# Kernel tuning notes

Hardware: AMD Instinct MI355X
Metric: run time of the kernel (lower is better)

## Reference

```python
import jax, jax.numpy as jnp
import numpy as np

N = 50000       # nodes
E = 1200000     # edges (before self-loops)
IN_CH = 128
HID = 64
L = 3           # FAConv layers
EPS_RES = 0.1   # FAConv eps residual weight
BN_EPS = 1e-5


def _bn(x, g, b):
    # BatchNorm1d, training-mode statistics (biased variance, like torch)
    mu = x.mean(axis=0)
    var = x.var(axis=0)
    return g * (x - mu) * jax.lax.rsqrt(var + BN_EPS) + b


def setup_inputs() -> dict:
    key = jax.random.key(0)
    ks = jax.random.split(key, 12)
    s = lambda d: 1.0 / np.sqrt(d)
    H2 = HID // 2
    return {
        "x": jax.random.normal(ks[0], (N, IN_CH), jnp.float32),
        "edge_index": jax.random.randint(ks[1], (2, E), 0, N, dtype=jnp.int32),
        "batch_size": 10000,
        "W_in": jax.random.normal(ks[2], (IN_CH, HID), jnp.float32) * s(IN_CH),
        "b_in": jnp.zeros((HID,), jnp.float32),
        "att_l": jax.random.normal(ks[3], (L, HID), jnp.float32) * s(HID),
        "att_r": jax.random.normal(ks[4], (L, HID), jnp.float32) * s(HID),
        "bn_g": jnp.ones((L, HID), jnp.float32),
        "bn_b": jnp.zeros((L, HID), jnp.float32),
        "W1": jax.random.normal(ks[5], (HID, HID), jnp.float32) * s(HID),
        "b1": jnp.zeros((HID,), jnp.float32),
        "g1": jnp.ones((HID,), jnp.float32),
        "be1": jnp.zeros((HID,), jnp.float32),
        "W2": jax.random.normal(ks[6], (HID, H2), jnp.float32) * s(HID),
        "b2": jnp.zeros((H2,), jnp.float32),
        "g2": jnp.ones((H2,), jnp.float32),
        "be2": jnp.zeros((H2,), jnp.float32),
        "W3": jax.random.normal(ks[7], (H2, 1), jnp.float32) * s(H2),
        "b3": jnp.zeros((1,), jnp.float32),
    }


def reference(x, edge_index, batch_size, W_in, b_in, att_l, att_r, bn_g, bn_b,
              W1, b1, g1, be1, W2, b2, g2, be2, W3, b3):
    n = x.shape[0]
    # gcn_norm with self-loops (same for all layers since graph is fixed)
    loops = jnp.arange(n, dtype=edge_index.dtype)
    src = jnp.concatenate([edge_index[0], loops])  # j (source)
    dst = jnp.concatenate([edge_index[1], loops])  # i (target)
    deg = jax.ops.segment_sum(jnp.ones_like(dst, dtype=x.dtype), dst, num_segments=n)
    dinv = jnp.where(deg > 0, jax.lax.rsqrt(deg), 0.0)
    norm = dinv[src] * dinv[dst]                   # [E+N]

    x0 = jax.nn.relu(x @ W_in + b_in)              # [N, HID]
    h = x0
    for l in range(L):
        al = h @ att_l[l]                          # [N] att_l^T x
        ar = h @ att_r[l]                          # [N] att_r^T x
        alpha = jnp.tanh(al[src] + ar[dst])        # [E+N] signed attention
        msg = h[src] * (alpha * norm)[:, None]     # gather + weight
        out = jax.ops.segment_sum(msg, dst, num_segments=n) + EPS_RES * x0
        h = _bn(jax.nn.relu(out), bn_g[l], bn_b[l])

    z = h[:batch_size]
    z = jax.nn.relu(_bn(z @ W1 + b1, g1, be1))
    z = jax.nn.relu(_bn(z @ W2 + b2, g2, be2))
    return (z @ W3 + b3).squeeze(-1)
```

## Files before the change

kernel.cpp:

```cpp
#include <hip/hip_runtime.h>
#include <hip/hip_bf16.h>
#include <math.h>

#define NND 50000
#define NE  1200000
#define TOT (NE + NND)
#define INCH 128
#define HID 64
#define H2  32
#define NL  3
#define BSZ 10000
#define NB  196
#define NHB 128
#define NSTAT 256
#define CHUNK 4096
#define EPS_RES 0.1f
#define BN_EPS 1e-5f

typedef unsigned short ushort8v __attribute__((ext_vector_type(8)));

__device__ __forceinline__ float b2f(unsigned short u) {
    return __uint_as_float((unsigned)u << 16);
}

__device__ __forceinline__ float fast_tanh(float x) {
    float cx = fminf(fmaxf(x, -8.f), 8.f);
    float e = __expf(2.f * cx);
    return 1.f - __fdividef(2.f, e + 1.f);
}


__global__ __launch_bounds__(256) void bhist_kernel(const int* __restrict__ dst, int* __restrict__ bh_part, int ne) {
    __shared__ int arr[256];
    arr[threadIdx.x] = 0;
    __syncthreads();
    int i = blockIdx.x * 256 + threadIdx.x;
    int stride = gridDim.x * 256;
    for (int e = i; e < ne; e += stride) atomicAdd(&arr[dst[e] >> 8], 1);
    __syncthreads();
    bh_part[blockIdx.x * 256 + threadIdx.x] = arr[threadIdx.x];
}

__global__ __launch_bounds__(256) void bscan_kernel(const int* __restrict__ bh_part,
                                                    int* __restrict__ bstart, int* __restrict__ bcur,
                                                    int* __restrict__ offsets) {
    __shared__ int ls[256];
    int t = threadIdx.x;
    int v = 0;
    for (int k = 0; k < NHB; k++) v += bh_part[k * 256 + t];
    ls[t] = v;
    __syncthreads();
    for (int off = 1; off < 256; off <<= 1) {
        int tv = (t >= off) ? ls[t - off] : 0;
        __syncthreads();
        ls[t] += tv;
        __syncthreads();
    }
    int excl = ls[t] - v;
    if (t < NB) { bstart[t] = excl; bcur[t] = excl; }
    if (t == NB) bstart[NB] = ls[NB - 1];
    if (t == 0) offsets[NND] = TOT;
}

__global__ __launch_bounds__(256) void passA_kernel(const int* __restrict__ src, const int* __restrict__ dst,
                                                    int* __restrict__ bcur, unsigned* __restrict__ ebuf, int ne) {
    __shared__ int arr[256];
    int t = threadIdx.x;
    int base = blockIdx.x * CHUNK;
    int lim = min(base + CHUNK, ne);
    arr[t] = 0;
    __syncthreads();
    for (int e = base + t; e < lim; e += 256) atomicAdd(&arr[dst[e] >> 8], 1);
    __syncthreads();
    int cnt_t = arr[t];
    int claimed = 0;
    if (cnt_t > 0) claimed = atomicAdd(&bcur[t], cnt_t);
    __syncthreads();
    arr[t] = claimed;
    __syncthreads();
    for (int e = base + t; e < lim; e += 256) {
        int d = dst[e];
        int pos = atomicAdd(&arr[d >> 8], 1);
        ebuf[pos] = ((unsigned)src[e] << 8) | (unsigned)(d & 255);
    }
}

__global__ __launch_bounds__(256) void bucket_build_kernel(const unsigned* __restrict__ ebuf, const int* __restrict__ bstart,
                                                           int* __restrict__ offsets, int* __restrict__ csr,
                                                           float* __restrict__ aldi_f) {
    __shared__ int dcnt[256];
    __shared__ int ls[256];
    __shared__ int cur[256];
    int b = blockIdx.x, t = threadIdx.x;
    dcnt[t] = 0;
    __syncthreads();
    int beg = bstart[b], end = bstart[b + 1];
    for (int p = beg + t; p < end; p += 256) atomicAdd(&dcnt[ebuf[p] & 255u], 1);
    __syncthreads();
    int node = b * 256 + t;
    bool valid = node < NND;
    int d = valid ? (dcnt[t] + 1) : 0;
    ls[t] = d;
    __syncthreads();
    for (int off = 1; off < 256; off <<= 1) {
        int tv = (t >= off) ? ls[t - off] : 0;
        __syncthreads();
        ls[t] += tv;
        __syncthreads();
    }
    int off = bstart[b] + b * 256 + ls[t] - d;
    if (valid) {
        offsets[node] = off;
        aldi_f[2 * node + 1] = rsqrtf((float)d);
        csr[off] = node;
        cur[t] = off + 1;
    }
    __syncthreads();
    for (int p = beg + t; p < end; p += 256) {
        unsigned ed = ebuf[p];
        int pos = atomicAdd(&cur[ed & 255u], 1);
        csr[pos] = (int)(ed >> 8);
    }
}

__global__ __launch_bounds__(256) void gemm_in_kernel(const float* __restrict__ x, const float* __restrict__ W,
                                                      const float* __restrict__ b,
                                                      const float* __restrict__ attl, const float* __restrict__ attr,
                                                      __hip_bfloat16* __restrict__ x0bf,
                                                      float* __restrict__ aldi_f, float* __restrict__ ar) {
    __shared__ float Wl[INCH * HID];
    __shared__ float xs[16 * INCH];
    int t = threadIdx.x;
    for (int i = t; i < INCH * HID; i += 256) Wl[i] = W[i];
    size_t rowbase = (size_t)blockIdx.x * 16;
    for (int i = t; i < 16 * INCH; i += 256) xs[i] = x[rowbase * INCH + i];
    __syncthreads();
    int col = t & 63, rg = t >> 6;
    float a0 = 0.f, a1 = 0.f, a2 = 0.f, a3 = 0.f;
    for (int k = 0; k < INCH; k++) {
        float wk = Wl[k * HID + col];
        a0 = fmaf(xs[(rg * 4 + 0) * INCH + k], wk, a0);
        a1 = fmaf(xs[(rg * 4 + 1) * INCH + k], wk, a1);
        a2 = fmaf(xs[(rg * 4 + 2) * INCH + k], wk, a2);
        a3 = fmaf(xs[(rg * 4 + 3) * INCH + k], wk, a3);
    }
    float bb = b[col];
    a0 = fmaxf(a0 + bb, 0.f); a1 = fmaxf(a1 + bb, 0.f);
    a2 = fmaxf(a2 + bb, 0.f); a3 = fmaxf(a3 + bb, 0.f);
    size_t r = rowbase + rg * 4;
    x0bf[(r + 0) * HID + col] = __float2bfloat16(a0);
    x0bf[(r + 1) * HID + col] = __float2bfloat16(a1);
    x0bf[(r + 2) * HID + col] = __float2bfloat16(a2);
    x0bf[(r + 3) * HID + col] = __float2bfloat16(a3);
    float wl = attl[col], wr = attr[col];
    float p0 = a0 * wl, q0 = a0 * wr, p1 = a1 * wl, q1 = a1 * wr;
    float p2 = a2 * wl, q2 = a2 * wr, p3 = a3 * wl, q3 = a3 * wr;
    for (int off = 32; off > 0; off >>= 1) {
        p0 += __shfl_xor(p0, off); q0 += __shfl_xor(q0, off);
        p1 += __shfl_xor(p1, off); q1 += __shfl_xor(q1, off);
        p2 += __shfl_xor(p2, off); q2 += __shfl_xor(q2, off);
        p3 += __shfl_xor(p3, off); q3 += __shfl_xor(q3, off);
    }
    if (col == 0) {
        aldi_f[2 * (r + 0)] = p0; ar[r + 0] = q0;
        aldi_f[2 * (r + 1)] = p1; ar[r + 1] = q1;
        aldi_f[2 * (r + 2)] = p2; ar[r + 2] = q2;
        aldi_f[2 * (r + 3)] = p3; ar[r + 3] = q3;
    }
}

__global__ __launch_bounds__(256) void aggregate_kernel(const __hip_bfloat16* __restrict__ hbf,
                                                        const __hip_bfloat16* __restrict__ x0bf,
                                                        const float2* __restrict__ aldi,
                                                        const float* __restrict__ ar,
                                                        const int* __restrict__ offsets, const int* __restrict__ csr,
                                                        float* __restrict__ y, int n) {
    int v = (blockIdx.x * 256 + threadIdx.x) >> 6;
    int lane = threadIdx.x & 63;
    if (v >= n) return;
    int g = lane >> 3;
    int cl = (lane & 7) << 3;
    int beg = offsets[v], end = offsets[v + 1];
    float arv = ar[v];
    const unsigned short* hb = (const unsigned short*)hbf;
    float a0 = 0.f, a1 = 0.f, a2 = 0.f, a3 = 0.f, a4 = 0.f, a5 = 0.f, a6 = 0.f, a7 = 0.f;
    for (int base = beg; base < end; base += 64) {
        int p = base + lane;
        int u = 0; float c = 0.f;
        if (p < end) {
            u = csr[p];
            float2 ad = aldi[u];
            c = fast_tanh(ad.x + arv) * ad.y;
        }
        int cnt = min(64, end - base);
        int nchunk = (cnt + 31) >> 5;
        for (int ch = 0; ch < nchunk; ++ch) {
            int j0 = (ch << 5) + g;
            int j1 = j0 + 8, j2 = j0 + 16, j3 = j0 + 24;
            int js0 = (j0 < cnt) ? j0 : 0;
            int js1 = (j1 < cnt) ? j1 : 0;
            int js2 = (j2 < cnt) ? j2 : 0;
            int js3 = (j3 < cnt) ? j3 : 0;
            int u0 = __shfl(u, js0); float c0 = __shfl(c, js0); if (j0 >= cnt) c0 = 0.f;
            int u1 = __shfl(u, js1); float c1 = __shfl(c, js1); if (j1 >= cnt) c1 = 0.f;
            int u2 = __shfl(u, js2); float c2 = __shfl(c, js2); if (j2 >= cnt) c2 = 0.f;
            int u3 = __shfl(u, js3); float c3 = __shfl(c, js3); if (j3 >= cnt) c3 = 0.f;
            ushort8v h0 = *(const ushort8v*)(hb + (size_t)u0 * HID + cl);
            ushort8v h1 = *(const ushort8v*)(hb + (size_t)u1 * HID + cl);
            ushort8v h2 = *(const ushort8v*)(hb + (size_t)u2 * HID + cl);
            ushort8v h3 = *(const ushort8v*)(hb + (size_t)u3 * HID + cl);
            a0 = fmaf(b2f(h0[0]), c0, a0); a1 = fmaf(b2f(h0[1]), c0, a1);
            a2 = fmaf(b2f(h0[2]), c0, a2); a3 = fmaf(b2f(h0[3]), c0, a3);
            a4 = fmaf(b2f(h0[4]), c0, a4); a5 = fmaf(b2f(h0[5]), c0, a5);
            a6 = fmaf(b2f(h0[6]), c0, a6); a7 = fmaf(b2f(h0[7]), c0, a7);
            a0 = fmaf(b2f(h1[0]), c1, a0); a1 = fmaf(b2f(h1[1]), c1, a1);
            a2 = fmaf(b2f(h1[2]), c1, a2); a3 = fmaf(b2f(h1[3]), c1, a3);
            a4 = fmaf(b2f(h1[4]), c1, a4); a5 = fmaf(b2f(h1[5]), c1, a5);
            a6 = fmaf(b2f(h1[6]), c1, a6); a7 = fmaf(b2f(h1[7]), c1, a7);
            a0 = fmaf(b2f(h2[0]), c2, a0); a1 = fmaf(b2f(h2[1]), c2, a1);
            a2 = fmaf(b2f(h2[2]), c2, a2); a3 = fmaf(b2f(h2[3]), c2, a3);
            a4 = fmaf(b2f(h2[4]), c2, a4); a5 = fmaf(b2f(h2[5]), c2, a5);
            a6 = fmaf(b2f(h2[6]), c2, a6); a7 = fmaf(b2f(h2[7]), c2, a7);
            a0 = fmaf(b2f(h3[0]), c3, a0); a1 = fmaf(b2f(h3[1]), c3, a1);
            a2 = fmaf(b2f(h3[2]), c3, a2); a3 = fmaf(b2f(h3[3]), c3, a3);
            a4 = fmaf(b2f(h3[4]), c3, a4); a5 = fmaf(b2f(h3[5]), c3, a5);
            a6 = fmaf(b2f(h3[6]), c3, a6); a7 = fmaf(b2f(h3[7]), c3, a7);
        }
    }
    for (int off = 8; off < 64; off <<= 1) {
        a0 += __shfl_xor(a0, off); a1 += __shfl_xor(a1, off);
        a2 += __shfl_xor(a2, off); a3 += __shfl_xor(a3, off);
        a4 += __shfl_xor(a4, off); a5 += __shfl_xor(a5, off);
        a6 += __shfl_xor(a6, off); a7 += __shfl_xor(a7, off);
    }
    if (g == 0) {
        float dv = aldi[v].y;
        ushort8v xb = *(const ushort8v*)((const unsigned short*)x0bf + (size_t)v * HID + cl);
        float4 o0, o1;
        o0.x = fmaxf(fmaf(EPS_RES, b2f(xb[0]), a0 * dv), 0.f);
        o0.y = fmaxf(fmaf(EPS_RES, b2f(xb[1]), a1 * dv), 0.f);
        o0.z = fmaxf(fmaf(EPS_RES, b2f(xb[2]), a2 * dv), 0.f);
        o0.w = fmaxf(fmaf(EPS_RES, b2f(xb[3]), a3 * dv), 0.f);
        o1.x = fmaxf(fmaf(EPS_RES, b2f(xb[4]), a4 * dv), 0.f);
        o1.y = fmaxf(fmaf(EPS_RES, b2f(xb[5]), a5 * dv), 0.f);
        o1.z = fmaxf(fmaf(EPS_RES, b2f(xb[6]), a6 * dv), 0.f);
        o1.w = fmaxf(fmaf(EPS_RES, b2f(xb[7]), a7 * dv), 0.f);
        *(float4*)(y + (size_t)v * HID + cl) = o0;
        *(float4*)(y + (size_t)v * HID + cl + 4) = o1;
    }
}

template <int C>
__global__ __launch_bounds__(256) void bn_stats_fused_kernel(const float* __restrict__ y, int rows,
                                                             const float* __restrict__ g, const float* __restrict__ b,
                                                             float rows_inv,
                                                             float* __restrict__ acc, int* __restrict__ counter,
                                                             float* __restrict__ scale, float* __restrict__ shift) {
    const int TPR = C / 4;
    const int RPW = 64 / TPR;
    int lane = threadIdx.x & 63;
    int wave = threadIdx.x >> 6;
    int cl = (lane % TPR) * 4;
    int rsub = lane / TPR;
    int rpb = 4 * RPW;
    int r = blockIdx.x * rpb + wave * RPW + rsub;
    int stride = gridDim.x * rpb;
    float s0 = 0.f, s1 = 0.f, s2 = 0.f, s3 = 0.f, q0 = 0.f, q1 = 0.f, q2 = 0.f, q3 = 0.f;
    for (; r < rows; r += stride) {
        float4 v = *(const float4*)(y + (size_t)r * C + cl);
        s0 += v.x; q0 = fmaf(v.x, v.x, q0);
        s1 += v.y; q1 = fmaf(v.y, v.y, q1);
        s2 += v.z; q2 = fmaf(v.z, v.z, q2);
        s3 += v.w; q3 = fmaf(v.w, v.w, q3);
    }
    for (int off = TPR; off < 64; off <<= 1) {
        s0 += __shfl_xor(s0, off); q0 += __shfl_xor(q0, off);
        s1 += __shfl_xor(s1, off); q1 += __shfl_xor(q1, off);
        s2 += __shfl_xor(s2, off); q2 += __shfl_xor(q2, off);
        s3 += __shfl_xor(s3, off); q3 += __shfl_xor(q3, off);
    }
    __shared__ float lsum[4][64], lsq[4][64];
    if (lane < TPR) {
        lsum[wave][cl + 0] = s0; lsq[wave][cl + 0] = q0;
        lsum[wave][cl + 1] = s1; lsq[wave][cl + 1] = q1;
        lsum[wave][cl + 2] = s2; lsq[wave][cl + 2] = q2;
        lsum[wave][cl + 3] = s3; lsq[wave][cl + 3] = q3;
    }
    __syncthreads();
    int t = threadIdx.x;
    if (t < C) {
        float ts = lsum[0][t] + lsum[1][t] + lsum[2][t] + lsum[3][t];
        float tq = lsq[0][t] + lsq[1][t] + lsq[2][t] + lsq[3][t];
        atomicAdd(&acc[t], ts);
        atomicAdd(&acc[64 + t], tq);
    }
    __shared__ int islast;
    __syncthreads();
    if (t == 0) {
        __threadfence();
        int old = atomicAdd(counter, 1);
        islast = (old == (int)gridDim.x - 1) ? 1 : 0;
    }
    __syncthreads();
    if (islast && t < C) {
        float ts = atomicAdd(&acc[t], 0.f);
        float tq = atomicAdd(&acc[64 + t], 0.f);
        float mean = ts * rows_inv;
        float var = tq * rows_inv - mean * mean;
        float sc = g[t] * rsqrtf(var + BN_EPS);
        scale[t] = sc;
        shift[t] = b[t] - mean * sc;
    }
}

__global__ __launch_bounds__(256) void bn_fused_apply_attn_kernel(const float* __restrict__ y, int rows,
                                                                  const float* __restrict__ g, const float* __restrict__ b,
                                                                  float rows_inv,
                                                                  float* __restrict__ acc, int* __restrict__ counter,
                                                                  const float* __restrict__ attl, const float* __restrict__ attr,
                                                                  __hip_bfloat16* __restrict__ hbf,
                                                                  float* __restrict__ aldi_f, float* __restrict__ ar) {
    const int TPR = 16;
    int lane = threadIdx.x & 63;
    int wave = threadIdx.x >> 6;
    int cl = (lane % TPR) * 4;
    int rsub = lane / TPR;
    int r = blockIdx.x * 16 + wave * 4 + rsub;
    int stride = gridDim.x * 16;
    float s0 = 0.f, s1 = 0.f, s2 = 0.f, s3 = 0.f, q0 = 0.f, q1 = 0.f, q2 = 0.f, q3 = 0.f;
    for (; r < rows; r += stride) {
        float4 v = *(const float4*)(y + (size_t)r * HID + cl);
        s0 += v.x; q0 = fmaf(v.x, v.x, q0);
        s1 += v.y; q1 = fmaf(v.y, v.y, q1);
        s2 += v.z; q2 = fmaf(v.z, v.z, q2);
        s3 += v.w; q3 = fmaf(v.w, v.w, q3);
    }
    for (int off = TPR; off < 64; off <<= 1) {
        s0 += __shfl_xor(s0, off); q0 += __shfl_xor(q0, off);
        s1 += __shfl_xor(s1, off); q1 += __shfl_xor(q1, off);
        s2 += __shfl_xor(s2, off); q2 += __shfl_xor(q2, off);
        s3 += __shfl_xor(s3, off); q3 += __shfl_xor(q3, off);
    }
    __shared__ float lsum[4][64], lsq[4][64];
    if (lane < TPR) {
        lsum[wave][cl + 0] = s0; lsq[wave][cl + 0] = q0;
        lsum[wave][cl + 1] = s1; lsq[wave][cl + 1] = q1;
        lsum[wave][cl + 2] = s2; lsq[wave][cl + 2] = q2;
        lsum[wave][cl + 3] = s3; lsq[wave][cl + 3] = q3;
    }
    __syncthreads();
    int t = threadIdx.x;
    if (t < 64) {
        float ts = lsum[0][t] + lsum[1][t] + lsum[2][t] + lsum[3][t];
        float tq = lsq[0][t] + lsq[1][t] + lsq[2][t] + lsq[3][t];
        atomicAdd(&acc[t], ts);
        atomicAdd(&acc[64 + t], tq);
    }
    __syncthreads();
    if (t == 0) {
        __threadfence();
        atomicAdd(counter, 1);
        while (atomicAdd(counter, 0) < (int)gridDim.x) {
            __builtin_amdgcn_s_sleep(2);
        }
    }
    __syncthreads();
    __shared__ float s_scale[64], s_shift[64];
    if (t < 64) {
        float ts = atomicAdd(&acc[t], 0.f);
        float tq = atomicAdd(&acc[64 + t], 0.f);
        float mean = ts * rows_inv;
        float var = tq * rows_inv - mean * mean;
        float sc = g[t] * rsqrtf(var + BN_EPS);
        s_scale[t] = sc;
        s_shift[t] = b[t] - mean * sc;
    }
    __syncthreads();
    float scl = s_scale[lane], shf = s_shift[lane];
    float wl = attl[lane], wr = attr[lane];
    for (int r0 = blockIdx.x * 16 + wave * 4; r0 < rows; r0 += stride) {
#pragma unroll
        for (int i = 0; i < 4; i++) {
            int rr = r0 + i;
            if (rr >= rows) break;
            float val = fmaf(y[(size_t)rr * HID + lane], scl, shf);
            hbf[(size_t)rr * HID + lane] = __float2bfloat16(val);
            float pl = val * wl;
            float pr = val * wr;
            for (int off = 32; off > 0; off >>= 1) {
                pl += __shfl_xor(pl, off);
                pr += __shfl_xor(pr, off);
            }
            if (lane == 0) { aldi_f[2 * rr] = pl; ar[rr] = pr; }
        }
    }
}

__global__ __launch_bounds__(256) void mlp1_kernel(const float* __restrict__ y, const float* __restrict__ scale,
                                                   const float* __restrict__ shift, const float* __restrict__ W,
                                                   const float* __restrict__ b, float* __restrict__ z1) {
    __shared__ float Wl[HID * HID];
    __shared__ float xs[16 * HID];
    int t = threadIdx.x;
    for (int i = t; i < HID * HID; i += 256) Wl[i] = W[i];
    size_t rowbase = (size_t)blockIdx.x * 16;
    for (int i = t; i < 16 * HID; i += 256) {
        int c = i & 63;
        xs[i] = fmaf(y[rowbase * HID + i], scale[c], shift[c]);
    }
    __syncthreads();
    int col = t & 63, rg = t >> 6;
    float a0 = 0.f, a1 = 0.f, a2 = 0.f, a3 = 0.f;
    for (int k = 0; k < HID; k++) {
        float wk = Wl[k * HID + col];
        a0 = fmaf(xs[(rg * 4 + 0) * HID + k], wk, a0);
        a1 = fmaf(xs[(rg * 4 + 1) * HID + k], wk, a1);
        a2 = fmaf(xs[(rg * 4 + 2) * HID + k], wk, a2);
        a3 = fmaf(xs[(rg * 4 + 3) * HID + k], wk, a3);
    }
    float bb = b[col];
    size_t r = rowbase + rg * 4;
    z1[(r + 0) * HID + col] = a0 + bb;
    z1[(r + 1) * HID + col] = a1 + bb;
    z1[(r + 2) * HID + col] = a2 + bb;
    z1[(r + 3) * HID + col] = a3 + bb;
}

__global__ __launch_bounds__(256) void mlp2_kernel(const float* __restrict__ z1, const float* __restrict__ scale,
                                                   const float* __restrict__ shift, const float* __restrict__ W,
                                                   const float* __restrict__ b, float* __restrict__ z2) {
    __shared__ float Wl[HID * H2];
    __shared__ float as[16 * HID];
    int t = threadIdx.x;
    for (int i = t; i < HID * H2; i += 256) Wl[i] = W[i];
    size_t rowbase = (size_t)blockIdx.x * 16;
    for (int i = t; i < 16 * HID; i += 256) {
        int c = i & 63;
        float v = z1[rowbase * HID + i];
        as[i] = fmaxf(fmaf(v, scale[c], shift[c]), 0.f);
    }
    __syncthreads();
    int col = t & 31, rg = t >> 5;
    float a0 = 0.f, a1 = 0.f;
    for (int k = 0; k < HID; k++) {
        float wk = Wl[k * H2 + col];
        a0 = fmaf(as[(rg * 2 + 0) * HID + k], wk, a0);
        a1 = fmaf(as[(rg * 2 + 1) * HID + k], wk, a1);
    }
    float bb = b[col];
    size_t r = rowbase + rg * 2;
    z2[(r + 0) * H2 + col] = a0 + bb;
    z2[(r + 1) * H2 + col] = a1 + bb;
}

__global__ __launch_bounds__(256) void mlp3_kernel(const float* __restrict__ z2, const float* __restrict__ scale,
                                                   const float* __restrict__ shift, const float* __restrict__ W3,
                                                   const float* __restrict__ b3, float* __restrict__ out, int rows) {
    int i = blockIdx.x * 256 + threadIdx.x;
    if (i >= rows) return;
    float acc = 0.f;
#pragma unroll
    for (int k = 0; k < H2; k++) {
        float v = fmaxf(fmaf(z2[(size_t)i * H2 + k], scale[k], shift[k]), 0.f);
        acc = fmaf(v, W3[k], acc);
    }
    out[i] = acc + b3[0];
}

extern "C" void kernel_launch(void* const* d_in, const int* in_sizes, int n_in,
                              void* d_out, int out_size, void* d_ws, size_t ws_size,
                              hipStream_t stream) {
    const float* x     = (const float*)d_in[0];
    const int*   ei    = (const int*)d_in[1];
    const int*   src   = ei;
    const int*   dst   = ei + NE;
    const float* W_in  = (const float*)d_in[3];
    const float* b_in  = (const float*)d_in[4];
    const float* att_l = (const float*)d_in[5];
    const float* att_r = (const float*)d_in[6];
    const float* bn_g  = (const float*)d_in[7];
    const float* bn_b  = (const float*)d_in[8];
    const float* W1    = (const float*)d_in[9];
    const float* b1    = (const float*)d_in[10];
    const float* g1    = (const float*)d_in[11];
    const float* be1   = (const float*)d_in[12];
    const float* W2    = (const float*)d_in[13];
    const float* b2    = (const float*)d_in[14];
    const float* g2    = (const float*)d_in[15];
    const float* be2   = (const float*)d_in[16];
    const float* W3    = (const float*)d_in[17];
    const float* b3    = (const float*)d_in[18];
    float* out = (float*)d_out;

    char* p = (char*)d_ws;
    auto carve = [&](size_t bytes) -> void* {
        void* r = (void*)p;
        p += (bytes + 255) & ~(size_t)255;
        return r;
    };
    int*   bh_part = (int*)carve((size_t)NHB * 256 * 4);
    int*   bstart  = (int*)carve(256 * 4);
    int*   bcur    = (int*)carve(256 * 4);
    int*   offsets = (int*)carve((size_t)(NND + 1) * 4);
    int*   csr     = (int*)carve((size_t)TOT * 4);
    float2* aldi   = (float2*)carve((size_t)NND * 8);
    float* ar      = (float*)carve((size_t)NND * 4);
    __hip_bfloat16* x0bf = (__hip_bfloat16*)carve((size_t)NND * HID * 2);
    __hip_bfloat16* hbfA = (__hip_bfloat16*)carve((size_t)NND * HID * 2);
    __hip_bfloat16* hbfB = (__hip_bfloat16*)carve((size_t)NND * HID * 2);
    float* ybuf    = (float*)carve((size_t)NND * HID * 4);
    unsigned* ebuf = (unsigned*)ybuf;
    float* accall  = (float*)carve(5 * 256 * 4);
    float* scale   = (float*)carve(64 * 4);
    float* shift   = (float*)carve(64 * 4);
    float* z1      = (float*)carve((size_t)BSZ * HID * 4);
    float* z2      = (float*)carve((size_t)BSZ * H2 * 4);

    auto accr = [&](int i) -> float* { return accall + i * 256; };
    auto ctr  = [&](int i) -> int*   { return (int*)(accall + i * 256 + 128); };

    const int nblkA = (NE + CHUNK - 1) / CHUNK;

    hipMemsetAsync(accall, 0, 5 * 256 * 4, stream);

    bhist_kernel<<<NHB, 256, 0, stream>>>(dst, bh_part, NE);
    gemm_in_kernel<<<NND / 16, 256, 0, stream>>>(x, W_in, b_in, att_l, att_r, x0bf, (float*)aldi, ar);
    bscan_kernel<<<1, 256, 0, stream>>>(bh_part, bstart, bcur, offsets);
    passA_kernel<<<nblkA, 256, 0, stream>>>(src, dst, bcur, ebuf, NE);
    bucket_build_kernel<<<NB, 256, 0, stream>>>(ebuf, bstart, offsets, csr, (float*)aldi);

    const __hip_bfloat16* h_in = x0bf;
    __hip_bfloat16* hbufs[2] = {hbfA, hbfB};
    for (int l = 0; l < NL; l++) {
        aggregate_kernel<<<NND / 4, 256, 0, stream>>>(h_in, x0bf, aldi, ar, offsets, csr, ybuf, NND);
        if (l < NL - 1) {
            bn_fused_apply_attn_kernel<<<NSTAT, 256, 0, stream>>>(ybuf, NND, bn_g + l * HID, bn_b + l * HID,
                                                                  1.0f / NND, accr(l), ctr(l),
                                                                  att_l + (l + 1) * HID, att_r + (l + 1) * HID,
                                                                  hbufs[l], (float*)aldi, ar);
            h_in = hbufs[l];
        } else {
            bn_stats_fused_kernel<64><<<NSTAT, 256, 0, stream>>>(ybuf, NND, bn_g + l * HID, bn_b + l * HID,
                                                                 1.0f / NND, accr(2), ctr(2), scale, shift);
        }
    }

    mlp1_kernel<<<BSZ / 16, 256, 0, stream>>>(ybuf, scale, shift, W1, b1, z1);
    bn_stats_fused_kernel<64><<<NSTAT, 256, 0, stream>>>(z1, BSZ, g1, be1, 1.0f / BSZ, accr(3), ctr(3), scale, shift);

    mlp2_kernel<<<BSZ / 16, 256, 0, stream>>>(z1, scale, shift, W2, b2, z2);
    bn_stats_fused_kernel<32><<<NSTAT, 256, 0, stream>>>(z2, BSZ, g2, be2, 1.0f / BSZ, accr(4), ctr(4), scale, shift);

    mlp3_kernel<<<(BSZ + 255) / 256, 256, 0, stream>>>(z2, scale, shift, W3, b3, out, BSZ);
}
```

Before: 396.6 us.

## Split fused BN grid-sync kernel into stats and apply kernels; persistent aggregate grid

Replaces the fused BN kernel, which spin-waited on a global atomic counter as a grid-wide barrier, with two launches: the last-block stats kernel writes scale and shift, then a separate full-grid apply kernel writes the bf16 features and the attention projections using vectorized float4 loads. The aggregate kernel becomes grid-stride over a fixed 2048 blocks, and the stats grid shrinks to 128 blocks. This removes the spin barrier and its poor parallelism in the apply phase, at the cost of an extra launch and a second read of y per layer.

```diff
diff --git a/kernel.cpp b/kernel.cpp
--- a/kernel.cpp
+++ b/kernel.cpp
@@ -12,12 +12,14 @@
 #define BSZ 10000
 #define NB  196
 #define NHB 128
-#define NSTAT 256
+#define NSTAT 128
+#define NAGG 2048
 #define CHUNK 4096
 #define EPS_RES 0.1f
 #define BN_EPS 1e-5f
 
 typedef unsigned short ushort8v __attribute__((ext_vector_type(8)));
+typedef unsigned short ushort4v __attribute__((ext_vector_type(4)));
 
 __device__ __forceinline__ float b2f(unsigned short u) {
     return __uint_as_float((unsigned)u << 16);
@@ -175,78 +177,81 @@
                                                         const float* __restrict__ ar,
                                                         const int* __restrict__ offsets, const int* __restrict__ csr,
                                                         float* __restrict__ y, int n) {
-    int v = (blockIdx.x * 256 + threadIdx.x) >> 6;
+    int wave = threadIdx.x >> 6;
     int lane = threadIdx.x & 63;
-    if (v >= n) return;
     int g = lane >> 3;
     int cl = (lane & 7) << 3;
-    int beg = offsets[v], end = offsets[v + 1];
-    float arv = ar[v];
     const unsigned short* hb = (const unsigned short*)hbf;
-    float a0 = 0.f, a1 = 0.f, a2 = 0.f, a3 = 0.f, a4 = 0.f, a5 = 0.f, a6 = 0.f, a7 = 0.f;
-    for (int base = beg; base < end; base += 64) {
-        int p = base + lane;
-        int u = 0; float c = 0.f;
-        if (p < end) {
-            u = csr[p];
-            float2 ad = aldi[u];
-            c = fast_tanh(ad.x + arv) * ad.y;
+    for (int vb = blockIdx.x; (vb << 2) < n; vb += gridDim.x) {
+        int v = (vb << 2) + wave;
+        if (v >= n) continue;
+        int beg = offsets[v], end = offsets[v + 1];
+        float arv = ar[v];
+        float a0 = 0.f, a1 = 0.f, a2 = 0.f, a3 = 0.f, a4 = 0.f, a5 = 0.f, a6 = 0.f, a7 = 0.f;
+        for (int base = beg; base < end; base += 64) {
+            int p = base + lane;
+            int u = 0; float c = 0.f;
+            if (p < end) {
+                u = csr[p];
+                float2 ad = aldi[u];
+                c = fast_tanh(ad.x + arv) * ad.y;
+            }
+            int cnt = min(64, end - base);
+            int nchunk = (cnt + 31) >> 5;
+            for (int ch = 0; ch < nchunk; ++ch) {
+                int j0 = (ch << 5) + g;
+                int j1 = j0 + 8, j2 = j0 + 16, j3 = j0 + 24;
+                int js0 = (j0 < cnt) ? j0 : 0;
+                int js1 = (j1 < cnt) ? j1 : 0;
+                int js2 = (j2 < cnt) ? j2 : 0;
+                int js3 = (j3 < cnt) ? j3 : 0;
+                int u0 = __shfl(u, js0); float c0 = __shfl(c, js0); if (j0 >= cnt) c0 = 0.f;
+                int u1 = __shfl(u, js1); float c1 = __shfl(c, js1); if (j1 >= cnt) c1 = 0.f;
+                int u2 = __shfl(u, js2); float c2 = __shfl(c, js2); if (j2 >= cnt) c2 = 0.f;
+                int u3 = __shfl(u, js3); float c3 = __shfl(c, js3); if (j3 >= cnt) c3 = 0.f;
+                ushort8v h0 = *(const ushort8v*)(hb + (size_t)u0 * HID + cl);
+                ushort8v h1 = *(const ushort8v*)(hb + (size_t)u1 * HID + cl);
+                ushort8v h2 = *(const ushort8v*)(hb + (size_t)u2 * HID + cl);
+                ushort8v h3 = *(const ushort8v*)(hb + (size_t)u3 * HID + cl);
+                a0 = fmaf(b2f(h0[0]), c0, a0); a1 = fmaf(b2f(h0[1]), c0, a1);
+                a2 = fmaf(b2f(h0[2]), c0, a2); a3 = fmaf(b2f(h0[3]), c0, a3);
+                a4 = fmaf(b2f(h0[4]), c0, a4); a5 = fmaf(b2f(h0[5]), c0, a5);
+                a6 = fmaf(b2f(h0[6]), c0, a6); a7 = fmaf(b2f(h0[7]), c0, a7);
+                a0 = fmaf(b2f(h1[0]), c1, a0); a1 = fmaf(b2f(h1[1]), c1, a1);
+                a2 = fmaf(b2f(h1[2]), c1, a2); a3 = fmaf(b2f(h1[3]), c1, a3);
+                a4 = fmaf(b2f(h1[4]), c1, a4); a5 = fmaf(b2f(h1[5]), c1, a5);
+                a6 = fmaf(b2f(h1[6]), c1, a6); a7 = fmaf(b2f(h1[7]), c1, a7);
+                a0 = fmaf(b2f(h2[0]), c2, a0); a1 = fmaf(b2f(h2[1]), c2, a1);
+                a2 = fmaf(b2f(h2[2]), c2, a2); a3 = fmaf(b2f(h2[3]), c2, a3);
+                a4 = fmaf(b2f(h2[4]), c2, a4); a5 = fmaf(b2f(h2[5]), c2, a5);
+                a6 = fmaf(b2f(h2[6]), c2, a6); a7 = fmaf(b2f(h2[7]), c2, a7);
+                a0 = fmaf(b2f(h3[0]), c3, a0); a1 = fmaf(b2f(h3[1]), c3, a1);
+                a2 = fmaf(b2f(h3[2]), c3, a2); a3 = fmaf(b2f(h3[3]), c3, a3);
+                a4 = fmaf(b2f(h3[4]), c3, a4); a5 = fmaf(b2f(h3[5]), c3, a5);
+                a6 = fmaf(b2f(h3[6]), c3, a6); a7 = fmaf(b2f(h3[7]), c3, a7);
+            }
         }
-        int cnt = min(64, end - base);
-        int nchunk = (cnt + 31) >> 5;
-        for (int ch = 0; ch < nchunk; ++ch) {
-            int j0 = (ch << 5) + g;
-            int j1 = j0 + 8, j2 = j0 + 16, j3 = j0 + 24;
-            int js0 = (j0 < cnt) ? j0 : 0;
-            int js1 = (j1 < cnt) ? j1 : 0;
-            int js2 = (j2 < cnt) ? j2 : 0;
-            int js3 = (j3 < cnt) ? j3 : 0;
-            int u0 = __shfl(u, js0); float c0 = __shfl(c, js0); if (j0 >= cnt) c0 = 0.f;
-            int u1 = __shfl(u, js1); float c1 = __shfl(c, js1); if (j1 >= cnt) c1 = 0.f;
-            int u2 = __shfl(u, js2); float c2 = __shfl(c, js2); if (j2 >= cnt) c2 = 0.f;
-            int u3 = __shfl(u, js3); float c3 = __shfl(c, js3); if (j3 >= cnt) c3 = 0.f;
-            ushort8v h0 = *(const ushort8v*)(hb + (size_t)u0 * HID + cl);
-            ushort8v h1 = *(const ushort8v*)(hb + (size_t)u1 * HID + cl);
-            ushort8v h2 = *(const ushort8v*)(hb + (size_t)u2 * HID + cl);
-            ushort8v h3 = *(const ushort8v*)(hb + (size_t)u3 * HID + cl);
-            a0 = fmaf(b2f(h0[0]), c0, a0); a1 = fmaf(b2f(h0[1]), c0, a1);
-            a2 = fmaf(b2f(h0[2]), c0, a2); a3 = fmaf(b2f(h0[3]), c0, a3);
-            a4 = fmaf(b2f(h0[4]), c0, a4); a5 = fmaf(b2f(h0[5]), c0, a5);
-            a6 = fmaf(b2f(h0[6]), c0, a6); a7 = fmaf(b2f(h0[7]), c0, a7);
-            a0 = fmaf(b2f(h1[0]), c1, a0); a1 = fmaf(b2f(h1[1]), c1, a1);
-            a2 = fmaf(b2f(h1[2]), c1, a2); a3 = fmaf(b2f(h1[3]), c1, a3);
-            a4 = fmaf(b2f(h1[4]), c1, a4); a5 = fmaf(b2f(h1[5]), c1, a5);
-            a6 = fmaf(b2f(h1[6]), c1, a6); a7 = fmaf(b2f(h1[7]), c1, a7);
-            a0 = fmaf(b2f(h2[0]), c2, a0); a1 = fmaf(b2f(h2[1]), c2, a1);
-            a2 = fmaf(b2f(h2[2]), c2, a2); a3 = fmaf(b2f(h2[3]), c2, a3);
-            a4 = fmaf(b2f(h2[4]), c2, a4); a5 = fmaf(b2f(h2[5]), c2, a5);
-            a6 = fmaf(b2f(h2[6]), c2, a6); a7 = fmaf(b2f(h2[7]), c2, a7);
-            a0 = fmaf(b2f(h3[0]), c3, a0); a1 = fmaf(b2f(h3[1]), c3, a1);
-            a2 = fmaf(b2f(h3[2]), c3, a2); a3 = fmaf(b2f(h3[3]), c3, a3);
-            a4 = fmaf(b2f(h3[4]), c3, a4); a5 = fmaf(b2f(h3[5]), c3, a5);
-            a6 = fmaf(b2f(h3[6]), c3, a6); a7 = fmaf(b2f(h3[7]), c3, a7);
+        for (int off = 8; off < 64; off <<= 1) {
+            a0 += __shfl_xor(a0, off); a1 += __shfl_xor(a1, off);
+            a2 += __shfl_xor(a2, off); a3 += __shfl_xor(a3, off);
+            a4 += __shfl_xor(a4, off); a5 += __shfl_xor(a5, off);
+            a6 += __shfl_xor(a6, off); a7 += __shfl_xor(a7, off);
         }
-    }
-    for (int off = 8; off < 64; off <<= 1) {
-        a0 += __shfl_xor(a0, off); a1 += __shfl_xor(a1, off);
-        a2 += __shfl_xor(a2, off); a3 += __shfl_xor(a3, off);
-        a4 += __shfl_xor(a4, off); a5 += __shfl_xor(a5, off);
-        a6 += __shfl_xor(a6, off); a7 += __shfl_xor(a7, off);
-    }
-    if (g == 0) {
-        float dv = aldi[v].y;
-        ushort8v xb = *(const ushort8v*)((const unsigned short*)x0bf + (size_t)v * HID + cl);
-        float4 o0, o1;
-        o0.x = fmaxf(fmaf(EPS_RES, b2f(xb[0]), a0 * dv), 0.f);
-        o0.y = fmaxf(fmaf(EPS_RES, b2f(xb[1]), a1 * dv), 0.f);
-        o0.z = fmaxf(fmaf(EPS_RES, b2f(xb[2]), a2 * dv), 0.f);
-        o0.w = fmaxf(fmaf(EPS_RES, b2f(xb[3]), a3 * dv), 0.f);
-        o1.x = fmaxf(fmaf(EPS_RES, b2f(xb[4]), a4 * dv), 0.f);
-        o1.y = fmaxf(fmaf(EPS_RES, b2f(xb[5]), a5 * dv), 0.f);
-        o1.z = fmaxf(fmaf(EPS_RES, b2f(xb[6]), a6 * dv), 0.f);
-        o1.w = fmaxf(fmaf(EPS_RES, b2f(xb[7]), a7 * dv), 0.f);
-        *(float4*)(y + (size_t)v * HID + cl) = o0;
-        *(float4*)(y + (size_t)v * HID + cl + 4) = o1;
+        if (g == 0) {
+            float dv = aldi[v].y;
+            ushort8v xb = *(const ushort8v*)((const unsigned short*)x0bf + (size_t)v * HID + cl);
+            float4 o0, o1;
+            o0.x = fmaxf(fmaf(EPS_RES, b2f(xb[0]), a0 * dv), 0.f);
+            o0.y = fmaxf(fmaf(EPS_RES, b2f(xb[1]), a1 * dv), 0.f);
+            o0.z = fmaxf(fmaf(EPS_RES, b2f(xb[2]), a2 * dv), 0.f);
+            o0.w = fmaxf(fmaf(EPS_RES, b2f(xb[3]), a3 * dv), 0.f);
+            o1.x = fmaxf(fmaf(EPS_RES, b2f(xb[4]), a4 * dv), 0.f);
+            o1.y = fmaxf(fmaf(EPS_RES, b2f(xb[5]), a5 * dv), 0.f);
+            o1.z = fmaxf(fmaf(EPS_RES, b2f(xb[6]), a6 * dv), 0.f);
+            o1.w = fmaxf(fmaf(EPS_RES, b2f(xb[7]), a7 * dv), 0.f);
+            *(float4*)(y + (size_t)v * HID + cl) = o0;
+            *(float4*)(y + (size_t)v * HID + cl + 4) = o1;
+        }
     }
 }
 
@@ -313,87 +318,39 @@
     }
 }
 
-__global__ __launch_bounds__(256) void bn_fused_apply_attn_kernel(const float* __restrict__ y, int rows,
-                                                                  const float* __restrict__ g, const float* __restrict__ b,
-                                                                  float rows_inv,
-                                                                  float* __restrict__ acc, int* __restrict__ counter,
-                                                                  const float* __restrict__ attl, const float* __restrict__ attr,
-                                                                  __hip_bfloat16* __restrict__ hbf,
-                                                                  float* __restrict__ aldi_f, float* __restrict__ ar) {
-    const int TPR = 16;
+__global__ __launch_bounds__(256) void bnapply_attn_kernel(const float* __restrict__ y, const float* __restrict__ scale,
+                                                           const float* __restrict__ shift,
+                                                           const float* __restrict__ attl, const float* __restrict__ attr,
+                                                           __hip_bfloat16* __restrict__ hbf,
+                                                           float* __restrict__ aldi_f, float* __restrict__ arr_out, int n) {
     int lane = threadIdx.x & 63;
     int wave = threadIdx.x >> 6;
-    int cl = (lane % TPR) * 4;
-    int rsub = lane / TPR;
+    int rsub = lane >> 4;
+    int cl = (lane & 15) << 2;
     int r = blockIdx.x * 16 + wave * 4 + rsub;
-    int stride = gridDim.x * 16;
-    float s0 = 0.f, s1 = 0.f, s2 = 0.f, s3 = 0.f, q0 = 0.f, q1 = 0.f, q2 = 0.f, q3 = 0.f;
-    for (; r < rows; r += stride) {
-        float4 v = *(const float4*)(y + (size_t)r * HID + cl);
-        s0 += v.x; q0 = fmaf(v.x, v.x, q0);
-        s1 += v.y; q1 = fmaf(v.y, v.y, q1);
-        s2 += v.z; q2 = fmaf(v.z, v.z, q2);
-        s3 += v.w; q3 = fmaf(v.w, v.w, q3);
-    }
-    for (int off = TPR; off < 64; off <<= 1) {
-        s0 += __shfl_xor(s0, off); q0 += __shfl_xor(q0, off);
-        s1 += __shfl_xor(s1, off); q1 += __shfl_xor(q1, off);
-        s2 += __shfl_xor(s2, off); q2 += __shfl_xor(q2, off);
-        s3 += __shfl_xor(s3, off); q3 += __shfl_xor(q3, off);
-    }
-    __shared__ float lsum[4][64], lsq[4][64];
-    if (lane < TPR) {
-        lsum[wave][cl + 0] = s0; lsq[wave][cl + 0] = q0;
-        lsum[wave][cl + 1] = s1; lsq[wave][cl + 1] = q1;
-        lsum[wave][cl + 2] = s2; lsq[wave][cl + 2] = q2;
-        lsum[wave][cl + 3] = s3; lsq[wave][cl + 3] = q3;
-    }
-    __syncthreads();
-    int t = threadIdx.x;
-    if (t < 64) {
-        float ts = lsum[0][t] + lsum[1][t] + lsum[2][t] + lsum[3][t];
-        float tq = lsq[0][t] + lsq[1][t] + lsq[2][t] + lsq[3][t];
-        atomicAdd(&acc[t], ts);
-        atomicAdd(&acc[64 + t], tq);
-    }
-    __syncthreads();
-    if (t == 0) {
-        __threadfence();
-        atomicAdd(counter, 1);
-        while (atomicAdd(counter, 0) < (int)gridDim.x) {
-            __builtin_amdgcn_s_sleep(2);
-        }
-    }
-    __syncthreads();
-    __shared__ float s_scale[64], s_shift[64];
-    if (t < 64) {
-        float ts = atomicAdd(&acc[t], 0.f);
-        float tq = atomicAdd(&acc[64 + t], 0.f);
-        float mean = ts * rows_inv;
-        float var = tq * rows_inv - mean * mean;
-        float sc = g[t] * rsqrtf(var + BN_EPS);
-        s_scale[t] = sc;
-        s_shift[t] = b[t] - mean * sc;
-    }
-    __syncthreads();
-    float scl = s_scale[lane], shf = s_shift[lane];
-    float wl = attl[lane], wr = attr[lane];
-    for (int r0 = blockIdx.x * 16 + wave * 4; r0 < rows; r0 += stride) {
-#pragma unroll
-        for (int i = 0; i < 4; i++) {
-            int rr = r0 + i;
-            if (rr >= rows) break;
-            float val = fmaf(y[(size_t)rr * HID + lane], scl, shf);
-            hbf[(size_t)rr * HID + lane] = __float2bfloat16(val);
-            float pl = val * wl;
-            float pr = val * wr;
-            for (int off = 32; off > 0; off >>= 1) {
-                pl += __shfl_xor(pl, off);
-                pr += __shfl_xor(pr, off);
-            }
-            if (lane == 0) { aldi_f[2 * rr] = pl; ar[rr] = pr; }
-        }
-    }
+    if (r >= n) return;
+    float4 v = *(const float4*)(y + (size_t)r * HID + cl);
+    float4 sc = *(const float4*)(scale + cl);
+    float4 sh = *(const float4*)(shift + cl);
+    float v0 = fmaf(v.x, sc.x, sh.x);
+    float v1 = fmaf(v.y, sc.y, sh.y);
+    float v2 = fmaf(v.z, sc.z, sh.z);
+    float v3 = fmaf(v.w, sc.w, sh.w);
+    __hip_bfloat16 b0 = __float2bfloat16(v0), b1 = __float2bfloat16(v1);
+    __hip_bfloat16 b2 = __float2bfloat16(v2), b3 = __float2bfloat16(v3);
+    ushort4v hv;
+    hv[0] = *(unsigned short*)&b0; hv[1] = *(unsigned short*)&b1;
+    hv[2] = *(unsigned short*)&b2; hv[3] = *(unsigned short*)&b3;
+    *(ushort4v*)((unsigned short*)hbf + (size_t)r * HID + cl) = hv;
+    float4 wl4 = *(const float4*)(attl + cl);
+    float4 wr4 = *(const float4*)(attr + cl);
+    float pl = v0 * wl4.x + v1 * wl4.y + v2 * wl4.z + v3 * wl4.w;
+    float pr = v0 * wr4.x + v1 * wr4.y + v2 * wr4.z + v3 * wr4.w;
+    for (int off = 1; off < 16; off <<= 1) {
+        pl += __shfl_xor(pl, off);
+        pr += __shfl_xor(pr, off);
+    }
+    if ((lane & 15) == 0) { aldi_f[2 * r] = pl; arr_out[r] = pr; }
 }
 
 __global__ __launch_bounds__(256) void mlp1_kernel(const float* __restrict__ y, const float* __restrict__ scale,
@@ -532,16 +489,14 @@
     const __hip_bfloat16* h_in = x0bf;
     __hip_bfloat16* hbufs[2] = {hbfA, hbfB};
     for (int l = 0; l < NL; l++) {
-        aggregate_kernel<<<NND / 4, 256, 0, stream>>>(h_in, x0bf, aldi, ar, offsets, csr, ybuf, NND);
+        aggregate_kernel<<<NAGG, 256, 0, stream>>>(h_in, x0bf, aldi, ar, offsets, csr, ybuf, NND);
+        bn_stats_fused_kernel<64><<<NSTAT, 256, 0, stream>>>(ybuf, NND, bn_g + l * HID, bn_b + l * HID,
+                                                             1.0f / NND, accr(l), ctr(l), scale, shift);
         if (l < NL - 1) {
-            bn_fused_apply_attn_kernel<<<NSTAT, 256, 0, stream>>>(ybuf, NND, bn_g + l * HID, bn_b + l * HID,
-                                                                  1.0f / NND, accr(l), ctr(l),
-                                                                  att_l + (l + 1) * HID, att_r + (l + 1) * HID,
-                                                                  hbufs[l], (float*)aldi, ar);
+            bnapply_attn_kernel<<<(NND + 15) / 16, 256, 0, stream>>>(ybuf, scale, shift,
+                                                                     att_l + (l + 1) * HID, att_r + (l + 1) * HID,
+                                                                     hbufs[l], (float*)aldi, ar, NND);
             h_in = hbufs[l];
-        } else {
-            bn_stats_fused_kernel<64><<<NSTAT, 256, 0, stream>>>(ybuf, NND, bn_g + l * HID, bn_b + l * HID,
-                                                                 1.0f / NND, accr(2), ctr(2), scale, shift);
         }
     }
 
```

After: 365.5 us. 7.8% less time.
